# Optimization experiments

Measured on AMD Instinct MI355X. Metric: run time of the kernel, lower is better.

Reference implementation:

```python
import jax, jax.numpy as jnp
from jax import lax
import numpy as np

KS, STRIDE, RATE, SCALE = 3, 1, 2, 10.0  # module init kwargs


def _resize_bilinear_ac(x, oh, ow):
    # F.interpolate(mode='bilinear', align_corners=True); x: [B,C,H,W]
    H, W = x.shape[2], x.shape[3]
    ys = jnp.linspace(0.0, H - 1.0, oh)
    xs = jnp.linspace(0.0, W - 1.0, ow)
    y0 = jnp.floor(ys).astype(jnp.int32)
    y1 = jnp.minimum(y0 + 1, H - 1)
    wy = (ys - y0)[:, None]
    x0 = jnp.floor(xs).astype(jnp.int32)
    x1 = jnp.minimum(x0 + 1, W - 1)
    wx = xs - x0
    g = lambda yi, xi: x[:, :, yi, :][:, :, :, xi]
    top = g(y0, x0) * (1 - wx) + g(y0, x1) * wx
    bot = g(y1, x0) * (1 - wx) + g(y1, x1) * wx
    return top * (1 - wy) + bot * wy


def _conv3x3(x, w, b):
    y = lax.conv_general_dilated(x, w, (1, 1), ((1, 1), (1, 1)),
                                 dimension_numbers=('NCHW', 'OIHW', 'NCHW'))
    return y + b[None, :, None, None]


def _extract_patches(x, k, s):
    # mirrors extract_patches(): ZeroPad2d(1) when k != 1, then unfold h,w
    if k != 1:
        x = jnp.pad(x, ((0, 0), (0, 0), (1, 1), (1, 1)))
    b, c, h, w = x.shape
    nh = (h - k) // s + 1
    nw = (w - k) // s + 1
    cols = jnp.stack([x[:, :, i:i + s * (nh - 1) + 1:s, j:j + s * (nw - 1) + 1:s]
                      for i in range(k) for j in range(k)], axis=-1)  # [B,C,nh,nw,k*k]
    return cols.reshape(b, c, nh, nw, k, k).transpose(0, 2, 3, 1, 4, 5).reshape(b, nh * nw, c, k, k)


def _instance_norm(x, eps=1e-5):
    mu = x.mean((2, 3), keepdims=True)
    var = ((x - mu) ** 2).mean((2, 3), keepdims=True)
    return (x - mu) * lax.rsqrt(var + eps)


def _conv_transpose(att, w):
    # torch F.conv_transpose2d(att, w, stride=2, padding=1); att [Q,h,w], w [Q,Cout,4,4]
    rhs = jnp.flip(w, (-2, -1)).transpose(1, 0, 2, 3)  # [Cout,Q,4,4]
    return lax.conv_general_dilated(att[None], rhs, (1, 1), ((2, 2), (2, 2)),
                                    lhs_dilation=(2, 2),
                                    dimension_numbers=('NCHW', 'OIHW', 'NCHW'))[0]


def _forward(background, foreground, mask, Wc, bc, Wm, bm, Wf, bf):
    h, w = foreground.shape[2], foreground.shape[3]
    mask64 = _resize_bilinear_ac(mask, h, w)
    fg_c = foreground * (1 - mask64)
    fg_m = foreground * mask64
    bg_c = background * (1 - mask64)
    bg_m = background * mask64
    # ODConv2d(fg, bg) stand-in: plain 3x3 conv on the fused features
    bg_c = _conv3x3(fg_c + bg_c, Wc, bc)
    bg_m = _conv3x3(fg_m + bg_m, Wm, bm)
    x = _conv3x3(bg_c + bg_m, Wf, bf)
    x = _instance_norm(x)
    x = x * jax.nn.sigmoid(x)  # MemoryEfficientSwish
    b = x.shape[0]
    raw_w = _extract_patches(x, 2 * RATE, STRIDE * RATE)       # [B,1024,256,4,4]
    x_down = _resize_bilinear_ac(x, h // RATE, w // RATE)       # [B,256,32,32]
    hd, wd = x_down.shape[2], x_down.shape[3]
    pt = _extract_patches(x_down, KS, STRIDE)                   # [B,1024,256,3,3]
    mask32 = _resize_bilinear_ac(mask64, hd, wd)
    mpt = _extract_patches(mask32, KS, STRIDE)                  # [B,1024,1,3,3]
    mm = (mpt.mean((2, 3, 4)) == 0.0).astype(x.dtype)[:, :, None, None]  # [B,1024,1,1]
    norm = jnp.sqrt((pt * pt).sum((2, 3, 4), keepdims=True))
    w_normed = pt / jnp.maximum(norm, 1e-4)
    # score = F.conv2d(x_down, w_normed, padding=1): batched patch-attention GEMM
    score = jnp.einsum('bqckl,bpckl->bqp', w_normed, pt).reshape(b, hd * wd, hd, wd)
    score = score * mm
    att = jax.nn.softmax(score * SCALE, axis=1) * mm
    att = jnp.clip(att, 1e-8, None)
    f1 = jax.vmap(_conv_transpose)(att, raw_w) / 4.0            # [B,256,64,64]
    return f1 * mask64 + x * (1 - mask64)


def setup_inputs() -> dict:
    key = jax.random.key(0)
    ks = jax.random.split(key, 9)
    B, C, H, W = 8, 256, 64, 64
    background = jax.random.normal(ks[0], (B, C, H, W), jnp.float32)
    foreground = jax.random.normal(ks[1], (B, C, H, W), jnp.float32)
    # blocky binary hole mask (16x16 blocks upsampled to 256x256)
    m0 = (jax.random.uniform(ks[2], (B, 1, 16, 16)) > 0.5).astype(jnp.float32)
    mask = jnp.repeat(jnp.repeat(m0, 16, axis=2), 16, axis=3)
    s = 0.05
    Wc = jax.random.normal(ks[3], (256, 256, 3, 3), jnp.float32) * s
    bc = jax.random.normal(ks[4], (256,), jnp.float32) * s
    Wm = jax.random.normal(ks[5], (256, 256, 3, 3), jnp.float32) * s
    bm = jax.random.normal(ks[6], (256,), jnp.float32) * s
    Wf = jax.random.normal(ks[7], (256, 256, 3, 3), jnp.float32) * s
    bf = jax.random.normal(ks[8], (256,), jnp.float32) * s
    return {'background': background, 'foreground': foreground, 'mask': mask,
            'Wc': Wc, 'bc': bc, 'Wm': Wm, 'bm': bm, 'Wf': Wf, 'bf': bf}


def reference(background, foreground, mask, Wc, bc, Wm, bm, Wf, bf):
    return _forward(background, foreground, mask, Wc, bc, Wm, bm, Wf, bf)
```

## Files before the change

### kernel.cpp

```cpp
#include <hip/hip_runtime.h>
#include <math.h>

#define B_ 8
#define C_ 256
#define NPIX 4096
#define NP 1024

typedef __attribute__((ext_vector_type(8))) short bf16x8;
typedef __attribute__((ext_vector_type(4))) float f32x4;

#define GLL16(src, dst) __builtin_amdgcn_global_load_lds( \
    (__attribute__((address_space(1))) void*)(src), \
    (__attribute__((address_space(3))) void*)(dst), 16, 0, 0)

__device__ __forceinline__ unsigned short f2bf(float f) {
  unsigned int u = __float_as_uint(f);
  unsigned int r = (u + 0x7FFFu + ((u >> 16) & 1u)) >> 16;
  return (unsigned short)r;
}
__device__ __forceinline__ unsigned int pk2(unsigned short lo, unsigned short hi) {
  return (unsigned int)lo | ((unsigned int)hi << 16);
}

__device__ __forceinline__ float wave_reduce_sum(float v) {
#pragma unroll
  for (int off = 32; off > 0; off >>= 1) v += __shfl_down(v, off, 64);
  return v;
}
__device__ __forceinline__ float wave_reduce_max(float v) {
#pragma unroll
  for (int off = 32; off > 0; off >>= 1) v = fmaxf(v, __shfl_down(v, off, 64));
  return v;
}

__global__ __launch_bounds__(256) void k_resize(const float* __restrict__ in, float* __restrict__ out,
                                                int IH, int IW, int OH, int OW, int nElem) {
  int idx = blockIdx.x * 256 + threadIdx.x;
  if (idx >= nElem) return;
  int ox = idx % OW; int t = idx / OW; int oy = t % OH; int bc = t / OH;
  float dy = (float)(IH - 1) / (float)(OH - 1);
  float dx = (float)(IW - 1) / (float)(OW - 1);
  float yf = (float)oy * dy;
  float xf = (float)ox * dx;
  float y0f = floorf(yf), x0f = floorf(xf);
  int y0 = (int)y0f, x0 = (int)x0f;
  int y1 = min(y0 + 1, IH - 1), x1 = min(x0 + 1, IW - 1);
  float wy = yf - y0f, wx = xf - x0f;
  const float* p = in + (size_t)bc * IH * IW;
  float a = p[y0 * IW + x0], b = p[y0 * IW + x1];
  float c = p[y1 * IW + x0], d = p[y1 * IW + x1];
  float top = a * (1.0f - wx) + b * wx;
  float bot = c * (1.0f - wx) + d * wx;
  out[idx] = top * (1.0f - wy) + bot * wy;
}

__global__ __launch_bounds__(256) void k_wprep(const float* __restrict__ Wc, const float* __restrict__ Wm,
                                               const float* __restrict__ Wf,
                                               unsigned short* __restrict__ Wp1, unsigned short* __restrict__ Wp2) {
  int idx = blockIdx.x * 256 + threadIdx.x;
  if (idx >= 3 * 589824) return;
  int part = idx / 589824;
  int rem = idx % 589824;
  int kk = rem >> 16, co = (rem >> 8) & 255, ci = rem & 255;
  const float* W = (part == 0) ? Wc : (part == 1) ? Wm : Wf;
  unsigned short o = f2bf(W[(size_t)co * 2304 + ci * 9 + kk]);
  if (part == 0) Wp1[rem] = o;
  else if (part == 1) Wp1[589824 + rem] = o;
  else Wp2[rem] = o;
}

__global__ __launch_bounds__(256) void k_bias(const float* __restrict__ bc, const float* __restrict__ bm,
                                              float* __restrict__ bias1, float* __restrict__ zpg) {
  int i = threadIdx.x;
  bias1[i] = bc[i] + bm[i];
  for (int j = i; j < 2048; j += 256) zpg[j] = 0.f;
}

__global__ __launch_bounds__(256) void k_prepAT(const float* __restrict__ fg, const float* __restrict__ bg,
                                                const float* __restrict__ m64,
                                                unsigned short* __restrict__ A0t, unsigned short* __restrict__ A1t) {
  __shared__ unsigned short T0[64][66];
  __shared__ unsigned short T1[64][66];
  int pt = blockIdx.x, ct = blockIdx.y, b = blockIdx.z;
  int pix0 = pt << 6, ci0 = ct << 6;
  int tid = threadIdx.x;
  {
    int r = tid >> 2, c4 = (tid & 3) << 4;
    size_t ib = (((size_t)(b * 256 + ci0 + r)) << 12) + pix0 + c4;
    const float* fb = fg + ib;
    const float* gb = bg + ib;
    const float* mb = m64 + (((size_t)b) << 12) + pix0 + c4;
#pragma unroll
    for (int k = 0; k < 16; k += 4) {
      float4 f = *(const float4*)(fb + k);
      float4 g = *(const float4*)(gb + k);
      float4 m = *(const float4*)(mb + k);
      float s0 = f.x + g.x, s1 = f.y + g.y, s2 = f.z + g.z, s3 = f.w + g.w;
      T0[r][c4 + k + 0] = f2bf(s0 * (1.f - m.x));
      T0[r][c4 + k + 1] = f2bf(s1 * (1.f - m.y));
      T0[r][c4 + k + 2] = f2bf(s2 * (1.f - m.z));
      T0[r][c4 + k + 3] = f2bf(s3 * (1.f - m.w));
      T1[r][c4 + k + 0] = f2bf(s0 * m.x);
      T1[r][c4 + k + 1] = f2bf(s1 * m.y);
      T1[r][c4 + k + 2] = f2bf(s2 * m.z);
      T1[r][c4 + k + 3] = f2bf(s3 * m.w);
    }
  }
  __syncthreads();
  {
    int pr = tid >> 2, cc = (tid & 3) << 4;
    unsigned int o0[8], o1[8];
#pragma unroll
    for (int k = 0; k < 8; k++) {
      o0[k] = pk2(T0[cc + 2 * k][pr], T0[cc + 2 * k + 1][pr]);
      o1[k] = pk2(T1[cc + 2 * k][pr], T1[cc + 2 * k + 1][pr]);
    }
    size_t ob = ((((size_t)b << 12) + pix0 + pr) << 8) + ci0 + cc;
    *(uint4*)&A0t[ob] = *(uint4*)&o0[0];
    *(uint4*)&A0t[ob + 8] = *(uint4*)&o0[4];
    *(uint4*)&A1t[ob] = *(uint4*)&o1[0];
    *(uint4*)&A1t[ob + 8] = *(uint4*)&o1[4];
  }
}

__device__ __forceinline__ int swz(int row, int slot) {
  return row * 32 + ((slot ^ (row & 3) ^ ((row >> 2) & 3)) << 3);
}

template <int NKK, bool OUT_TRANS_BF16>
__global__ __launch_bounds__(256, 2) void k_conv2ph(const unsigned short* __restrict__ A0t,
                                                    const unsigned short* __restrict__ A1t,
                                                    const unsigned short* __restrict__ Wp,
                                                    const float* __restrict__ bias,
                                                    const unsigned short* __restrict__ zp,
                                                    void* __restrict__ outp) {
  __shared__ __align__(16) unsigned short AB[2][8192];
  int wgl = blockIdx.x + 32 * (blockIdx.y + 2 * blockIdx.z);
  int nid = (wgl & 7) * 64 + (wgl >> 3);
  int bp = nid & 31, cot = (nid >> 5) & 1, b = nid >> 6;
  int tid = threadIdx.x, lane = tid & 63, w3 = tid >> 6;
  int wm = w3 >> 1, wn = w3 & 1;

  int rA = w3 * 32 + (lane >> 2), rA1 = rA + 16;
  int ds0 = (lane & 3) ^ (rA & 3) ^ ((rA >> 2) & 3);
  int ds1 = (lane & 3) ^ (rA1 & 3) ^ ((rA1 >> 2) & 3);
  int y_0 = bp * 2 + (rA >> 6), x_0 = rA & 63;
  int y_1 = bp * 2 + (rA1 >> 6), x_1 = rA1 & 63;
  int co_0 = cot * 128 + rA, co_1 = cot * 128 + rA1;

  f32x4 acc[4][4];
#pragma unroll
  for (int i = 0; i < 4; i++)
#pragma unroll
    for (int j = 0; j < 4; j++) acc[i][j] = (f32x4){0.f, 0.f, 0.f, 0.f};

  const unsigned short *pA0, *pA1, *pB0, *pB1;

#define UPDATE(kkv) {                                                           \
    int kk_ = (kkv);                                                            \
    int kw_ = (NKK == 18 && kk_ >= 9) ? kk_ - 9 : kk_;                          \
    const unsigned short* Asrc_ = (NKK == 18 && kk_ >= 9) ? A1t : A0t;          \
    int ky_ = kw_ / 3 - 1, kx_ = kw_ % 3 - 1;                                   \
    int yy0_ = y_0 + ky_, xx0_ = x_0 + kx_;                                     \
    int yy1_ = y_1 + ky_, xx1_ = x_1 + kx_;                                     \
    pA0 = ((unsigned)yy0_ < 64u && (unsigned)xx0_ < 64u)                        \
        ? Asrc_ + ((((size_t)(b << 6) + yy0_) << 6) + xx0_) * 256 + ds0 * 8     \
        : zp + ds0 * 8;                                                         \
    pA1 = ((unsigned)yy1_ < 64u && (unsigned)xx1_ < 64u)                        \
        ? Asrc_ + ((((size_t)(b << 6) + yy1_) << 6) + xx1_) * 256 + ds1 * 8     \
        : zp + ds1 * 8;                                                         \
    pB0 = Wp + ((size_t)kk_ << 16) + co_0 * 256 + ds0 * 8;                      \
    pB1 = Wp + ((size_t)kk_ << 16) + co_1 * 256 + ds1 * 8;                      \
  }
#define STAGE(c2, buf) {                                                        \
    int ci0_ = ((c2) & 7) << 5;                                                 \
    unsigned short* lb_ = &AB[buf][0];                                          \
    GLL16(pA0 + ci0_, lb_ + w3 * 1024);                                         \
    GLL16(pA1 + ci0_, lb_ + w3 * 1024 + 512);                                   \
    GLL16(pB0 + ci0_, lb_ + 4096 + w3 * 1024);                                  \
    GLL16(pB1 + ci0_, lb_ + 4096 + w3 * 1024 + 512);                            \
  }

  const int NCH = NKK * 8;
  UPDATE(0);
  STAGE(0, 0);
  for (int c = 0; c < NCH; ++c) {
    asm volatile("" ::: "memory");
    __builtin_amdgcn_s_barrier();
    asm volatile("" ::: "memory");
    if (c < NCH - 1) {
      int cn = c + 1;
      if ((cn & 7) == 0) UPDATE(cn >> 3);
      STAGE(cn, cn & 1);
      asm volatile("s_waitcnt vmcnt(4)" ::: "memory");
    } else {
      asm volatile("s_waitcnt vmcnt(0)" ::: "memory");
    }
    __builtin_amdgcn_s_barrier();
    asm volatile("" ::: "memory");
    const unsigned short* Al = &AB[c & 1][0];
    const unsigned short* Bl = &AB[c & 1][4096];
    int slot = lane >> 4;
    int mr = wm * 64 + (lane & 15), ncc = wn * 64 + (lane & 15);
    bf16x8 af[4], bfr[4];
#pragma unroll
    for (int i = 0; i < 4; i++) af[i] = *(const bf16x8*)&Al[swz(mr + i * 16, slot)];
#pragma unroll
    for (int j = 0; j < 4; j++) bfr[j] = *(const bf16x8*)&Bl[swz(ncc + j * 16, slot)];
#pragma unroll
    for (int i = 0; i < 4; i++)
#pragma unroll
      for (int j = 0; j < 4; j++)
        acc[i][j] = __builtin_amdgcn_mfma_f32_16x16x32_bf16(af[i], bfr[j], acc[i][j], 0, 0, 0);
  }
#undef STAGE
#undef UPDATE

  int px0 = bp * 128 + wm * 64 + ((lane >> 4) << 2);
  int co0 = cot * 128 + wn * 64 + (lane & 15);
#pragma unroll
  for (int j = 0; j < 4; j++) {
    int co = co0 + j * 16;
    float bs = bias[co];
#pragma unroll
    for (int i = 0; i < 4; i++) {
#pragma unroll
      for (int r = 0; r < 4; r++) {
        float v = acc[i][j][r] + bs;
        int pix = px0 + i * 16 + r;
        if (OUT_TRANS_BF16)
          ((unsigned short*)outp)[((((size_t)b << 12) + pix) << 8) + co] = f2bf(v);
        else
          ((float*)outp)[((((size_t)b << 8) + co) << 12) + pix] = v;
      }
    }
  }
}

__global__ __launch_bounds__(256) void k_innorm(float* __restrict__ x) {
  __shared__ float s4[4];
  int bc = blockIdx.x;
  float* p = x + (size_t)bc * NPIX;
  int tid = threadIdx.x;
  int lane = tid & 63, w = tid >> 6;
  float v[16];
  float s = 0.f;
#pragma unroll
  for (int i = 0; i < 16; i++) { v[i] = p[tid + i * 256]; s += v[i]; }
  s = wave_reduce_sum(s);
  if (lane == 0) s4[w] = s;
  __syncthreads();
  float mean = (s4[0] + s4[1] + s4[2] + s4[3]) * (1.0f / 4096.0f);
  __syncthreads();
  float s2 = 0.f;
#pragma unroll
  for (int i = 0; i < 16; i++) { float d = v[i] - mean; s2 += d * d; }
  s2 = wave_reduce_sum(s2);
  if (lane == 0) s4[w] = s2;
  __syncthreads();
  float var = (s4[0] + s4[1] + s4[2] + s4[3]) * (1.0f / 4096.0f);
  float inv = 1.0f / sqrtf(var + 1e-5f);
#pragma unroll
  for (int i = 0; i < 16; i++) {
    float xn = (v[i] - mean) * inv;
    float sg = 1.0f / (1.0f + expf(-xn));
    p[tid + i * 256] = xn * sg;
  }
}

__global__ __launch_bounds__(256) void k_trans_xd(const float* __restrict__ xd,
                                                  unsigned short* __restrict__ xdt) {
  __shared__ unsigned short T[64][66];
  int qt = blockIdx.x, ct = blockIdx.y, b = blockIdx.z;
  int q0 = qt << 6, ci0 = ct << 6;
  int tid = threadIdx.x;
  {
    int r = tid >> 2, c4 = (tid & 3) << 4;
    const float* xb = xd + (((size_t)(b * 256 + ci0 + r)) << 10) + q0 + c4;
#pragma unroll
    for (int k = 0; k < 16; k += 4) {
      float4 f = *(const float4*)(xb + k);
      T[r][c4 + k + 0] = f2bf(f.x);
      T[r][c4 + k + 1] = f2bf(f.y);
      T[r][c4 + k + 2] = f2bf(f.z);
      T[r][c4 + k + 3] = f2bf(f.w);
    }
  }
  __syncthreads();
  {
    int qr = tid >> 2, cc = (tid & 3) << 4;
    unsigned int o[8];
#pragma unroll
    for (int k = 0; k < 8; k++) o[k] = pk2(T[cc + 2 * k][qr], T[cc + 2 * k + 1][qr]);
    size_t ob = ((((size_t)b << 10) + q0 + qr) << 8) + ci0 + cc;
    *(uint4*)&xdt[ob] = *(uint4*)&o[0];
    *(uint4*)&xdt[ob + 8] = *(uint4*)&o[4];
  }
}

__global__ __launch_bounds__(256) void k_sq32(const float* __restrict__ xd, float* __restrict__ sq) {
  int idx = blockIdx.x * 256 + threadIdx.x;
  if (idx >= B_ * NP) return;
  int pix = idx & 1023; int b = idx >> 10;
  const float* p = xd + (size_t)b * C_ * NP + pix;
  float s = 0.f;
  for (int c = 0; c < C_; c++) { float v = p[c * NP]; s += v * v; }
  sq[idx] = s;
}

__global__ __launch_bounds__(256) void k_normmm(const float* __restrict__ sq, const float* __restrict__ m32,
                                                float* __restrict__ fq) {
  int idx = blockIdx.x * 256 + threadIdx.x;
  if (idx >= B_ * NP) return;
  int q = idx & 1023, b = idx >> 10;
  int qi = q >> 5, qj = q & 31;
  float ns = 0.f, ms = 0.f;
#pragma unroll
  for (int k = 0; k < 3; k++)
#pragma unroll
    for (int l = 0; l < 3; l++) {
      int r = qi + k - 1, c = qj + l - 1;
      if (r >= 0 && r < 32 && c >= 0 && c < 32) {
        ns += sq[b * NP + r * 32 + c];
        ms += m32[b * NP + r * 32 + c];
      }
    }
  float f = (ms == 0.0f) ? (1.0f / fmaxf(sqrtf(ns), 1e-4f)) : 0.0f;
  fq[idx] = f;
}

__global__ __launch_bounds__(256, 2) void k_gram2ph(const unsigned short* __restrict__ xdt,
                                                    const float* __restrict__ fq,
                                                    const unsigned short* __restrict__ zp,
                                                    float* __restrict__ sc) {
  __shared__ __align__(16) unsigned short AB[2][8192];
  int wgl = blockIdx.x + 8 * (blockIdx.y + 8 * blockIdx.z);
  int nid = (wgl & 7) * 64 + (wgl >> 3);
  int bp = nid & 7, bq = (nid >> 3) & 7, b = nid >> 6;
  int tid = threadIdx.x, lane = tid & 63, w3 = tid >> 6;
  int wm = w3 >> 1, wn = w3 & 1;

  int rA = w3 * 32 + (lane >> 2), rA1 = rA + 16;
  int ds0 = (lane & 3) ^ (rA & 3) ^ ((rA >> 2) & 3);
  int ds1 = (lane & 3) ^ (rA1 & 3) ^ ((rA1 >> 2) & 3);
  int pA0r = bp * 128 + rA, pA1r = bp * 128 + rA1;
  int pB0r = bq * 128 + rA, pB1r = bq * 128 + rA1;
  int piA0 = pA0r >> 5, pjA0 = pA0r & 31, piA1 = pA1r >> 5, pjA1 = pA1r & 31;
  int piB0 = pB0r >> 5, pjB0 = pB0r & 31, piB1 = pB1r >> 5, pjB1 = pB1r & 31;
  const unsigned short* xb = xdt + (((size_t)b) << 18);

  f32x4 acc[4][4];
#pragma unroll
  for (int i = 0; i < 4; i++)
#pragma unroll
    for (int j = 0; j < 4; j++) acc[i][j] = (f32x4){0.f, 0.f, 0.f, 0.f};

  const unsigned short *pA0, *pA1, *pB0, *pB1;

#define GUPDATE(kkv) {                                                          \
    int kk_ = (kkv);                                                            \
    int dy_ = kk_ / 3 - 1, dx_ = kk_ % 3 - 1;                                   \
    int ya0 = piA0 + dy_, xa0 = pjA0 + dx_;                                     \
    int ya1 = piA1 + dy_, xa1 = pjA1 + dx_;                                     \
    int yb0 = piB0 + dy_, xb0 = pjB0 + dx_;                                     \
    int yb1 = piB1 + dy_, xb1 = pjB1 + dx_;                                     \
    pA0 = ((unsigned)ya0 < 32u && (unsigned)xa0 < 32u)                          \
        ? xb + ((((size_t)ya0 << 5) + xa0) << 8) + ds0 * 8 : zp + ds0 * 8;      \
    pA1 = ((unsigned)ya1 < 32u && (unsigned)xa1 < 32u)                          \
        ? xb + ((((size_t)ya1 << 5) + xa1) << 8) + ds1 * 8 : zp + ds1 * 8;      \
    pB0 = ((unsigned)yb0 < 32u && (unsigned)xb0 < 32u)                          \
        ? xb + ((((size_t)yb0 << 5) + xb0) << 8) + ds0 * 8 : zp + ds0 * 8;      \
    pB1 = ((unsigned)yb1 < 32u && (unsigned)xb1 < 32u)                          \
        ? xb + ((((size_t)yb1 << 5) + xb1) << 8) + ds1 * 8 : zp + ds1 * 8;      \
  }
#define GSTAGE(c2, buf) {                                                       \
    int ci0_ = ((c2) & 7) << 5;                                                 \
    unsigned short* lb_ = &AB[buf][0];                                          \
    GLL16(pA0 + ci0_, lb_ + w3 * 1024);                                         \
    GLL16(pA1 + ci0_, lb_ + w3 * 1024 + 512);                                   \
    GLL16(pB0 + ci0_, lb_ + 4096 + w3 * 1024);                                  \
    GLL16(pB1 + ci0_, lb_ + 4096 + w3 * 1024 + 512);                            \
  }

  GUPDATE(0);
  GSTAGE(0, 0);
  for (int c = 0; c < 72; ++c) {
    asm volatile("" ::: "memory");
    __builtin_amdgcn_s_barrier();
    asm volatile("" ::: "memory");
    if (c < 71) {
      int cn = c + 1;
      if ((cn & 7) == 0) GUPDATE(cn >> 3);
      GSTAGE(cn, cn & 1);
      asm volatile("s_waitcnt vmcnt(4)" ::: "memory");
    } else {
      asm volatile("s_waitcnt vmcnt(0)" ::: "memory");
    }
    __builtin_amdgcn_s_barrier();
    asm volatile("" ::: "memory");
    const unsigned short* Al = &AB[c & 1][0];
    const unsigned short* Bl = &AB[c & 1][4096];
    int slot = lane >> 4;
    int mr = wm * 64 + (lane & 15), ncc = wn * 64 + (lane & 15);
    bf16x8 af[4], bfr[4];
#pragma unroll
    for (int i = 0; i < 4; i++) af[i] = *(const bf16x8*)&Al[swz(mr + i * 16, slot)];
#pragma unroll
    for (int j = 0; j < 4; j++) bfr[j] = *(const bf16x8*)&Bl[swz(ncc + j * 16, slot)];
#pragma unroll
    for (int i = 0; i < 4; i++)
#pragma unroll
      for (int j = 0; j < 4; j++)
        acc[i][j] = __builtin_amdgcn_mfma_f32_16x16x32_bf16(af[i], bfr[j], acc[i][j], 0, 0, 0);
  }
#undef GSTAGE
#undef GUPDATE

  int q0 = bq * 128 + wn * 64 + (lane & 15);
  int p0 = bp * 128 + wm * 64 + ((lane >> 4) << 2);
#pragma unroll
  for (int j = 0; j < 4; j++) {
    int q = q0 + j * 16;
    float f = fq[(b << 10) + q];
#pragma unroll
    for (int i = 0; i < 4; i++)
#pragma unroll
      for (int r = 0; r < 4; r++)
        sc[((size_t)(b << 10) + (p0 + i * 16 + r)) * NP + q] = acc[i][j][r] * f;
  }
}

__global__ __launch_bounds__(256) void k_softmax(const float* __restrict__ sc, const float* __restrict__ fq,
                                                 unsigned short* __restrict__ attb) {
  __shared__ float s4[4];
  int row = blockIdx.x;
  int b = row >> 10;
  const float* r = sc + (size_t)row * NP;
  int tid = threadIdx.x;
  int lane = tid & 63, w = tid >> 6;
  float4 sv = *(const float4*)&r[tid * 4];
  float l0 = sv.x * 10.f, l1 = sv.y * 10.f, l2 = sv.z * 10.f, l3 = sv.w * 10.f;
  float mx = fmaxf(fmaxf(l0, l1), fmaxf(l2, l3));
  mx = wave_reduce_max(mx);
  if (lane == 0) s4[w] = mx;
  __syncthreads();
  float M = fmaxf(fmaxf(s4[0], s4[1]), fmaxf(s4[2], s4[3]));
  __syncthreads();
  float e0 = expf(l0 - M), e1 = expf(l1 - M), e2 = expf(l2 - M), e3 = expf(l3 - M);
  float s = e0 + e1 + e2 + e3;
  s = wave_reduce_sum(s);
  if (lane == 0) s4[w] = s;
  __syncthreads();
  float inv = 1.0f / (s4[0] + s4[1] + s4[2] + s4[3]);
  const float* fb = fq + b * NP + tid * 4;
  float m0 = fb[0] > 0.f ? 1.f : 0.f;
  float m1 = fb[1] > 0.f ? 1.f : 0.f;
  float m2 = fb[2] > 0.f ? 1.f : 0.f;
  float m3 = fb[3] > 0.f ? 1.f : 0.f;
  float a0 = fmaxf(e0 * inv * m0, 1e-8f);
  float a1 = fmaxf(e1 * inv * m1, 1e-8f);
  float a2 = fmaxf(e2 * inv * m2, 1e-8f);
  float a3 = fmaxf(e3 * inv * m3, 1e-8f);
  uint2 o;
  o.x = pk2(f2bf(a0), f2bf(a1));
  o.y = pk2(f2bf(a2), f2bf(a3));
  *(uint2*)&attb[(size_t)row * NP + tid * 4] = o;
}

__global__ __launch_bounds__(256) void k_xprep(const float* __restrict__ x,
                                               unsigned short* __restrict__ P0,
                                               unsigned short* __restrict__ P1,
                                               unsigned short* __restrict__ P2) {
  int idx = blockIdx.x * 256 + threadIdx.x;
  int xh8 = idx & 3;
  int yh = (idx >> 2) & 31;
  int co = (idx >> 7) & 255;
  int pc = (idx >> 15) & 3;
  int b  = idx >> 17;
  int cy = pc >> 1, cx = pc & 1;
  const float* row = x + ((size_t)(b * 256 + co) * 64 + (2 * yh + cy)) * 64 + 16 * xh8;
  float4 f0 = *(const float4*)(row);
  float4 f1 = *(const float4*)(row + 4);
  float4 f2 = *(const float4*)(row + 8);
  float4 f3 = *(const float4*)(row + 12);
  unsigned short v0 = f2bf(cx ? f0.y : f0.x), v1 = f2bf(cx ? f0.w : f0.z);
  unsigned short v2 = f2bf(cx ? f1.y : f1.x), v3 = f2bf(cx ? f1.w : f1.z);
  unsigned short v4 = f2bf(cx ? f2.y : f2.x), v5 = f2bf(cx ? f2.w : f2.z);
  unsigned short v6 = f2bf(cx ? f3.y : f3.x), v7 = f2bf(cx ? f3.w : f3.z);
  int prev = __shfl_up((int)v7, 1, 64);
  int next = __shfl_down((int)v0, 1, 64);
  unsigned short pv = (xh8 == 0) ? (unsigned short)0 : (unsigned short)prev;
  unsigned short nx = (xh8 == 3) ? (unsigned short)0 : (unsigned short)next;
  size_t base = ((size_t)((b * 4 + pc) * 256 + co) * 32 + yh) * 32 + 8 * xh8;
  uint4 w0 = {pk2(v0, v1), pk2(v2, v3), pk2(v4, v5), pk2(v6, v7)};
  *(uint4*)&P0[base] = w0;
  uint4 w1 = {pk2(pv, v0), pk2(v1, v2), pk2(v3, v4), pk2(v5, v6)};
  *(uint4*)&P1[base] = w1;
  uint4 w2 = {pk2(v1, v2), pk2(v3, v4), pk2(v5, v6), pk2(v7, nx)};
  *(uint4*)&P2[base] = w2;
}

__global__ __launch_bounds__(256, 2) void k_pv(const unsigned short* __restrict__ attb,
                                               const unsigned short* __restrict__ P0,
                                               const unsigned short* __restrict__ P1,
                                               const unsigned short* __restrict__ P2,
                                               const unsigned short* __restrict__ zp,
                                               const float* __restrict__ xbuf,
                                               const float* __restrict__ m64,
                                               float* __restrict__ out) {
  __shared__ __align__(16) unsigned short AB[2][8192];
  int wg = blockIdx.x + blockIdx.y * 8 + blockIdx.z * 16;
  int nid = (wg & 7) * 64 + (wg >> 3);
  int bn = nid & 7, bm = (nid >> 3) & 1, z = nid >> 4;
  int b = z >> 2, cls = z & 3, cy = cls >> 1, cx = cls & 1;
  int tid = threadIdx.x, lane = tid & 63, w3 = tid >> 6;
  int wm = w3 >> 1, wn = w3 & 1;

  int dy1 = cy ? -1 : 1;
  int pio1 = cy ? 1 : -1;
  int pjo1 = cx ? 1 : -1;
  const unsigned short* Pdx = cx ? P1 : P2;

  int rA0 = w3 * 32 + (lane >> 2);
  int rA1 = rA0 + 16;
  int ds0 = (lane & 3) ^ (rA0 & 3) ^ ((rA0 >> 2) & 3);
  int ds1 = (lane & 3) ^ (rA1 & 3) ^ ((rA1 >> 2) & 3);
  int offA0 = ((z * 256 + bm * 128 + rA0) << 10) + ds0 * 8;
  int offA1 = ((z * 256 + bm * 128 + rA1) << 10) + ds1 * 8;

  const unsigned short* attB = attb + ((size_t)b << 20);
  int o0 = bn * 128 + rA0, o1 = bn * 128 + rA1;
  int oy0 = o0 >> 5, ox0 = o0 & 31, oy1 = o1 >> 5, ox1 = o1 & 31;
#define BPTR(oyv, oxv, dsv, tyv, txv) ({                                        \
    int pi = (oyv) + ((tyv) ? pio1 : 0);                                        \
    int pj = (oxv) + ((txv) ? pjo1 : 0);                                        \
    (pi >= 0 && pi < 32 && pj >= 0 && pj < 32)                                  \
        ? attB + (((pi << 5) + pj) << 10) + (dsv) * 8 : zp; })
  const unsigned short* b0t0 = BPTR(oy0, ox0, ds0, 0, 0);
  const unsigned short* b0t1 = BPTR(oy0, ox0, ds0, 0, 1);
  const unsigned short* b0t2 = BPTR(oy0, ox0, ds0, 1, 0);
  const unsigned short* b0t3 = BPTR(oy0, ox0, ds0, 1, 1);
  const unsigned short* b1t0 = BPTR(oy1, ox1, ds1, 0, 0);
  const unsigned short* b1t1 = BPTR(oy1, ox1, ds1, 0, 1);
  const unsigned short* b1t2 = BPTR(oy1, ox1, ds1, 1, 0);
  const unsigned short* b1t3 = BPTR(oy1, ox1, ds1, 1, 1);
#undef BPTR

  f32x4 acc[4][4];
#pragma unroll
  for (int i = 0; i < 4; i++)
#pragma unroll
    for (int j = 0; j < 4; j++) acc[i][j] = (f32x4){0.f, 0.f, 0.f, 0.f};

  int dA0 = w3 * 1024, dA1 = w3 * 1024 + 512;
  int dB0 = 4096 + w3 * 1024, dB1 = 4096 + w3 * 1024 + 512;

#define PSTAGE(c2, buf) {                                                       \
    int t2 = (c2) >> 5, qi = (c2) & 31;                                         \
    int q32 = qi * 32;                                                          \
    const unsigned short* Ab = (t2 & 1) ? Pdx : P0;                             \
    int dyo = (t2 >> 1) ? dy1 * 32 : 0;                                         \
    bool vA = (t2 < 2) || ((dy1 > 0) ? (qi < 31) : (qi > 0));                   \
    if (!vA) Ab = zp;                                                           \
    int oA0 = vA ? offA0 + dyo + q32 : 0;                                       \
    int oA1 = vA ? offA1 + dyo + q32 : 0;                                       \
    unsigned short* lb = &AB[buf][0];                                           \
    GLL16(Ab + oA0, lb + dA0);                                                  \
    GLL16(Ab + oA1, lb + dA1);                                                  \
    const unsigned short* sB0 = (t2 == 0 ? b0t0 : t2 == 1 ? b0t1 : t2 == 2 ? b0t2 : b0t3) + q32; \
    const unsigned short* sB1 = (t2 == 0 ? b1t0 : t2 == 1 ? b1t1 : t2 == 2 ? b1t2 : b1t3) + q32; \
    GLL16(sB0, lb + dB0);                                                       \
    GLL16(sB1, lb + dB1);                                                       \
  }

  PSTAGE(0, 0);
  for (int c = 0; c < 128; ++c) {
    asm volatile("" ::: "memory");
    __builtin_amdgcn_s_barrier();
    asm volatile("" ::: "memory");
    if (c < 127) {
      PSTAGE(c + 1, (c + 1) & 1);
      asm volatile("s_waitcnt vmcnt(4)" ::: "memory");
    } else {
      asm volatile("s_waitcnt vmcnt(0)" ::: "memory");
    }
    __builtin_amdgcn_s_barrier();
    asm volatile("" ::: "memory");
    const unsigned short* Al = &AB[c & 1][0];
    const unsigned short* Bl = &AB[c & 1][4096];
    int slot = lane >> 4;
    int mr = wm * 64 + (lane & 15), ncc = wn * 64 + (lane & 15);
    bf16x8 af[4], bfr[4];
#pragma unroll
    for (int i = 0; i < 4; i++) af[i] = *(const bf16x8*)&Al[swz(mr + i * 16, slot)];
#pragma unroll
    for (int j = 0; j < 4; j++) bfr[j] = *(const bf16x8*)&Bl[swz(ncc + j * 16, slot)];
#pragma unroll
    for (int i = 0; i < 4; i++)
#pragma unroll
      for (int j = 0; j < 4; j++)
        acc[i][j] = __builtin_amdgcn_mfma_f32_16x16x32_bf16(af[i], bfr[j], acc[i][j], 0, 0, 0);
  }
#undef PSTAGE

  int co0 = bm * 128 + wm * 64 + ((lane >> 4) << 2);
  int oo0 = bn * 128 + wn * 64 + (lane & 15);
#pragma unroll
  for (int j = 0; j < 4; j++) {
    int o = oo0 + j * 16;
    int oy = ((o >> 5) << 1) + cy, ox = ((o & 31) << 1) + cx;
    int opix = oy * 64 + ox;
    float msk = m64[b * NPIX + opix];
    float s = 0.25f * msk, t1m = 1.0f - msk;
#pragma unroll
    for (int i = 0; i < 4; i++) {
#pragma unroll
      for (int r = 0; r < 4; r++) {
        int co = co0 + i * 16 + r;
        size_t xi = (size_t)(b * C_ + co) * NPIX + opix;
        out[xi] = acc[i][j][r] * s + xbuf[xi] * t1m;
      }
    }
  }
}

extern "C" void kernel_launch(void* const* d_in, const int* in_sizes, int n_in,
                              void* d_out, int out_size, void* d_ws, size_t ws_size,
                              hipStream_t stream) {
  const float* bg   = (const float*)d_in[0];
  const float* fg   = (const float*)d_in[1];
  const float* mask = (const float*)d_in[2];
  const float* Wc   = (const float*)d_in[3];
  const float* bc   = (const float*)d_in[4];
  const float* Wm   = (const float*)d_in[5];
  const float* bm   = (const float*)d_in[6];
  const float* Wf   = (const float*)d_in[7];
  const float* bf   = (const float*)d_in[8];
  float* out = (float*)d_out;
  float* w = (float*)d_ws;

  float* mask64 = w;
  float* mask32 = w + 32768;
  float* sq32   = w + 40960;
  float* fq     = w + 49152;
  float* bias1  = w + 57344;
  float* zpage  = w + 57600;
  unsigned short* A0t = (unsigned short*)(w + 65536);
  unsigned short* A1t = (unsigned short*)(w + 65536 + 4194304);
  float* sc = w + 65536;
  unsigned short* P0u = (unsigned short*)(w + 65536);
  unsigned short* P1u = (unsigned short*)(w + 4259840);
  unsigned short* tbuf_t = (unsigned short*)(w + 8454144);
  float* xd = w + 8454144;
  unsigned short* xdt = (unsigned short*)(w + 10551296);
  unsigned short* attb = (unsigned short*)(w + 8454144);
  float* xbuf = w + 12648448;
  unsigned short* Wp1 = (unsigned short*)(w + 21037056);
  unsigned short* Wp2 = (unsigned short*)(w + 21626880);
  unsigned short* P2u = (unsigned short*)(w + 21037056);

  const unsigned short* zp = (const unsigned short*)zpage;

  hipLaunchKernelGGL(k_resize, dim3(128), dim3(256), 0, stream, mask, mask64, 256, 256, 64, 64, 32768);
  hipLaunchKernelGGL(k_wprep, dim3(6912), dim3(256), 0, stream, Wc, Wm, Wf, Wp1, Wp2);
  hipLaunchKernelGGL(k_bias, dim3(1), dim3(256), 0, stream, bc, bm, bias1, zpage);
  hipLaunchKernelGGL(k_prepAT, dim3(64, 4, 8), dim3(256), 0, stream, fg, bg, mask64, A0t, A1t);
  hipLaunchKernelGGL((k_conv2ph<18, true>), dim3(32, 2, 8), dim3(256), 0, stream,
                     A0t, A1t, Wp1, bias1, zp, (void*)tbuf_t);
  hipLaunchKernelGGL((k_conv2ph<9, false>), dim3(32, 2, 8), dim3(256), 0, stream,
                     tbuf_t, tbuf_t, Wp2, bf, zp, (void*)xbuf);
  hipLaunchKernelGGL(k_innorm, dim3(B_ * C_), dim3(256), 0, stream, xbuf);
  hipLaunchKernelGGL(k_resize, dim3(8192), dim3(256), 0, stream, xbuf, xd, 64, 64, 32, 32, B_ * C_ * NP);
  hipLaunchKernelGGL(k_resize, dim3(32), dim3(256), 0, stream, mask64, mask32, 64, 64, 32, 32, B_ * NP);
  hipLaunchKernelGGL(k_trans_xd, dim3(16, 4, 8), dim3(256), 0, stream, xd, xdt);
  hipLaunchKernelGGL(k_sq32, dim3(32), dim3(256), 0, stream, xd, sq32);
  hipLaunchKernelGGL(k_normmm, dim3(32), dim3(256), 0, stream, sq32, mask32, fq);
  hipLaunchKernelGGL(k_gram2ph, dim3(8, 8, 8), dim3(256), 0, stream, xdt, fq, zp, sc);
  hipLaunchKernelGGL(k_softmax, dim3(B_ * NP), dim3(256), 0, stream, sc, fq, attb);
  hipLaunchKernelGGL(k_xprep, dim3(4096), dim3(256), 0, stream, xbuf, P0u, P1u, P2u);
  hipLaunchKernelGGL(k_pv, dim3(8, 2, 32), dim3(256), 0, stream, attb, P0u, P1u, P2u,
                     zp, xbuf, mask64, out);
}
```

Before: 356.1 us.

## Enlarge MFMA GEMM tiles to 256x128 and fuse norm with downsample

The conv, gram and PV GEMM kernels now use 256x128 output tiles, with 8x4 MFMA accumulators per wave and larger LDS stages, in place of 128x128. This halves the workgroup count and raises operand reuse per LDS load. The instance-norm kernel now also does the 64->32 bilinear downsample from shared memory, and the mask downsample is folded into the fq kernel, which removes two launches and one pass over memory. The cost is higher register pressure and fewer workgroups, 256 per GEMM, which may underfill the GPU's compute units.

```diff
diff --git a/kernel.cpp b/kernel.cpp
--- a/kernel.cpp
+++ b/kernel.cpp
@@ -12,6 +12,8 @@
 #define GLL16(src, dst) __builtin_amdgcn_global_load_lds( \
     (__attribute__((address_space(1))) void*)(src), \
     (__attribute__((address_space(3))) void*)(dst), 16, 0, 0)
+
+#define MFMA16(a, b, c) __builtin_amdgcn_mfma_f32_16x16x32_bf16((a), (b), (c), 0, 0, 0)
 
 __device__ __forceinline__ unsigned short f2bf(float f) {
   unsigned int u = __float_as_uint(f);
@@ -127,103 +129,114 @@
   return row * 32 + ((slot ^ (row & 3) ^ ((row >> 2) & 3)) << 3);
 }
 
+
 template <int NKK, bool OUT_TRANS_BF16>
-__global__ __launch_bounds__(256, 2) void k_conv2ph(const unsigned short* __restrict__ A0t,
-                                                    const unsigned short* __restrict__ A1t,
-                                                    const unsigned short* __restrict__ Wp,
-                                                    const float* __restrict__ bias,
-                                                    const unsigned short* __restrict__ zp,
-                                                    void* __restrict__ outp) {
-  __shared__ __align__(16) unsigned short AB[2][8192];
-  int wgl = blockIdx.x + 32 * (blockIdx.y + 2 * blockIdx.z);
-  int nid = (wgl & 7) * 64 + (wgl >> 3);
-  int bp = nid & 31, cot = (nid >> 5) & 1, b = nid >> 6;
+__global__ __launch_bounds__(256, 2) void k_conv3(const unsigned short* __restrict__ A0t,
+                                                  const unsigned short* __restrict__ A1t,
+                                                  const unsigned short* __restrict__ Wp,
+                                                  const float* __restrict__ bias,
+                                                  const unsigned short* __restrict__ zp,
+                                                  void* __restrict__ outp) {
+  __shared__ __align__(16) unsigned short AB[2][12288];
+  int wgl = blockIdx.x;
+  int nid = (wgl & 7) * 32 + (wgl >> 3);
+  int bp = nid & 15, cot = (nid >> 4) & 1, b = nid >> 5;
   int tid = threadIdx.x, lane = tid & 63, w3 = tid >> 6;
   int wm = w3 >> 1, wn = w3 & 1;
 
-  int rA = w3 * 32 + (lane >> 2), rA1 = rA + 16;
-  int ds0 = (lane & 3) ^ (rA & 3) ^ ((rA >> 2) & 3);
-  int ds1 = (lane & 3) ^ (rA1 & 3) ^ ((rA1 >> 2) & 3);
-  int y_0 = bp * 2 + (rA >> 6), x_0 = rA & 63;
-  int y_1 = bp * 2 + (rA1 >> 6), x_1 = rA1 & 63;
-  int co_0 = cot * 128 + rA, co_1 = cot * 128 + rA1;
-
-  f32x4 acc[4][4];
-#pragma unroll
-  for (int i = 0; i < 4; i++)
+  int r0 = w3 * 32 + (lane >> 2), r1 = r0 + 16;
+  int ds0 = (lane & 3) ^ (r0 & 3) ^ ((r0 >> 2) & 3);
+  int ds1 = (lane & 3) ^ (r1 & 3) ^ ((r1 >> 2) & 3);
+  int y0r = bp * 4 + (r0 >> 6), x0r = r0 & 63;
+  int y1r = bp * 4 + (r1 >> 6), x1r = r1 & 63;
+  int y2r = bp * 4 + ((r0 + 128) >> 6), x2r = x0r;
+  int y3r = bp * 4 + ((r1 + 128) >> 6), x3r = x1r;
+  int rb0 = w3 * 16 + (lane >> 2);
+  int dsb = (lane & 3) ^ (rb0 & 3) ^ ((rb0 >> 2) & 3);
+  int cob0 = cot * 128 + rb0, cob1 = cob0 + 64;
+
+  f32x4 acc[8][4];
+#pragma unroll
+  for (int i = 0; i < 8; i++)
 #pragma unroll
     for (int j = 0; j < 4; j++) acc[i][j] = (f32x4){0.f, 0.f, 0.f, 0.f};
 
-  const unsigned short *pA0, *pA1, *pB0, *pB1;
-
-#define UPDATE(kkv) {                                                           \
+  const unsigned short *pA0, *pA1, *pA2, *pA3, *pB0, *pB1;
+#define UPD(kkv) {                                                              \
     int kk_ = (kkv);                                                            \
     int kw_ = (NKK == 18 && kk_ >= 9) ? kk_ - 9 : kk_;                          \
     const unsigned short* Asrc_ = (NKK == 18 && kk_ >= 9) ? A1t : A0t;          \
     int ky_ = kw_ / 3 - 1, kx_ = kw_ % 3 - 1;                                   \
-    int yy0_ = y_0 + ky_, xx0_ = x_0 + kx_;                                     \
-    int yy1_ = y_1 + ky_, xx1_ = x_1 + kx_;                                     \
-    pA0 = ((unsigned)yy0_ < 64u && (unsigned)xx0_ < 64u)                        \
-        ? Asrc_ + ((((size_t)(b << 6) + yy0_) << 6) + xx0_) * 256 + ds0 * 8     \
-        : zp + ds0 * 8;                                                         \
-    pA1 = ((unsigned)yy1_ < 64u && (unsigned)xx1_ < 64u)                        \
-        ? Asrc_ + ((((size_t)(b << 6) + yy1_) << 6) + xx1_) * 256 + ds1 * 8     \
-        : zp + ds1 * 8;                                                         \
-    pB0 = Wp + ((size_t)kk_ << 16) + co_0 * 256 + ds0 * 8;                      \
-    pB1 = Wp + ((size_t)kk_ << 16) + co_1 * 256 + ds1 * 8;                      \
+    int yy, xx;                                                                 \
+    yy = y0r + ky_; xx = x0r + kx_;                                             \
+    pA0 = ((unsigned)yy < 64u && (unsigned)xx < 64u)                            \
+        ? Asrc_ + ((((size_t)(b << 6) + yy) << 6) + xx) * 256 + ds0 * 8 : zp + ds0 * 8; \
+    yy = y1r + ky_; xx = x1r + kx_;                                             \
+    pA1 = ((unsigned)yy < 64u && (unsigned)xx < 64u)                            \
+        ? Asrc_ + ((((size_t)(b << 6) + yy) << 6) + xx) * 256 + ds1 * 8 : zp + ds1 * 8; \
+    yy = y2r + ky_; xx = x2r + kx_;                                             \
+    pA2 = ((unsigned)yy < 64u && (unsigned)xx < 64u)                            \
+        ? Asrc_ + ((((size_t)(b << 6) + yy) << 6) + xx) * 256 + ds0 * 8 : zp + ds0 * 8; \
+    yy = y3r + ky_; xx = x3r + kx_;                                             \
+    pA3 = ((unsigned)yy < 64u && (unsigned)xx < 64u)                            \
+        ? Asrc_ + ((((size_t)(b << 6) + yy) << 6) + xx) * 256 + ds1 * 8 : zp + ds1 * 8; \
+    pB0 = Wp + ((size_t)kk_ << 16) + (size_t)cob0 * 256 + dsb * 8;              \
+    pB1 = Wp + ((size_t)kk_ << 16) + (size_t)cob1 * 256 + dsb * 8;              \
   }
 #define STAGE(c2, buf) {                                                        \
     int ci0_ = ((c2) & 7) << 5;                                                 \
     unsigned short* lb_ = &AB[buf][0];                                          \
     GLL16(pA0 + ci0_, lb_ + w3 * 1024);                                         \
     GLL16(pA1 + ci0_, lb_ + w3 * 1024 + 512);                                   \
-    GLL16(pB0 + ci0_, lb_ + 4096 + w3 * 1024);                                  \
-    GLL16(pB1 + ci0_, lb_ + 4096 + w3 * 1024 + 512);                            \
+    GLL16(pA2 + ci0_, lb_ + 4096 + w3 * 1024);                                  \
+    GLL16(pA3 + ci0_, lb_ + 4096 + w3 * 1024 + 512);                            \
+    GLL16(pB0 + ci0_, lb_ + 8192 + w3 * 512);                                   \
+    GLL16(pB1 + ci0_, lb_ + 8192 + 2048 + w3 * 512);                            \
   }
 
   const int NCH = NKK * 8;
-  UPDATE(0);
+  UPD(0);
   STAGE(0, 0);
+  int slot = lane >> 4;
+  int mr = wm * 128 + (lane & 15), ncc = wn * 64 + (lane & 15);
   for (int c = 0; c < NCH; ++c) {
     asm volatile("" ::: "memory");
     __builtin_amdgcn_s_barrier();
     asm volatile("" ::: "memory");
     if (c < NCH - 1) {
       int cn = c + 1;
-      if ((cn & 7) == 0) UPDATE(cn >> 3);
+      if ((cn & 7) == 0) UPD(cn >> 3);
       STAGE(cn, cn & 1);
-      asm volatile("s_waitcnt vmcnt(4)" ::: "memory");
+      asm volatile("s_waitcnt vmcnt(6)" ::: "memory");
     } else {
       asm volatile("s_waitcnt vmcnt(0)" ::: "memory");
     }
     __builtin_amdgcn_s_barrier();
     asm volatile("" ::: "memory");
     const unsigned short* Al = &AB[c & 1][0];
-    const unsigned short* Bl = &AB[c & 1][4096];
-    int slot = lane >> 4;
-    int mr = wm * 64 + (lane & 15), ncc = wn * 64 + (lane & 15);
-    bf16x8 af[4], bfr[4];
-#pragma unroll
-    for (int i = 0; i < 4; i++) af[i] = *(const bf16x8*)&Al[swz(mr + i * 16, slot)];
+    const unsigned short* Bl = &AB[c & 1][8192];
+    bf16x8 af[8], bfr[4];
+#pragma unroll
+    for (int i = 0; i < 8; i++) af[i] = *(const bf16x8*)&Al[swz(mr + i * 16, slot)];
 #pragma unroll
     for (int j = 0; j < 4; j++) bfr[j] = *(const bf16x8*)&Bl[swz(ncc + j * 16, slot)];
 #pragma unroll
-    for (int i = 0; i < 4; i++)
+    for (int i = 0; i < 8; i++)
 #pragma unroll
       for (int j = 0; j < 4; j++)
-        acc[i][j] = __builtin_amdgcn_mfma_f32_16x16x32_bf16(af[i], bfr[j], acc[i][j], 0, 0, 0);
+        acc[i][j] = MFMA16(af[i], bfr[j], acc[i][j]);
   }
 #undef STAGE
-#undef UPDATE
-
-  int px0 = bp * 128 + wm * 64 + ((lane >> 4) << 2);
+#undef UPD
+
+  int px0 = bp * 256 + wm * 128 + ((lane >> 4) << 2);
   int co0 = cot * 128 + wn * 64 + (lane & 15);
 #pragma unroll
   for (int j = 0; j < 4; j++) {
     int co = co0 + j * 16;
     float bs = bias[co];
 #pragma unroll
-    for (int i = 0; i < 4; i++) {
+    for (int i = 0; i < 8; i++) {
 #pragma unroll
       for (int r = 0; r < 4; r++) {
         float v = acc[i][j][r] + bs;
@@ -237,7 +250,8 @@
   }
 }
 
-__global__ __launch_bounds__(256) void k_innorm(float* __restrict__ x) {
+__global__ __launch_bounds__(256) void k_post(float* __restrict__ x, float* __restrict__ xd) {
+  __shared__ float sL[4096];
   __shared__ float s4[4];
   int bc = blockIdx.x;
   float* p = x + (size_t)bc * NPIX;
@@ -264,7 +278,28 @@
   for (int i = 0; i < 16; i++) {
     float xn = (v[i] - mean) * inv;
     float sg = 1.0f / (1.0f + expf(-xn));
-    p[tid + i * 256] = xn * sg;
+    float o = xn * sg;
+    p[tid + i * 256] = o;
+    sL[tid + i * 256] = o;
+  }
+  __syncthreads();
+  float dyx = 63.0f / 31.0f;
+  float* xdp = xd + (size_t)bc * NP;
+#pragma unroll
+  for (int k = 0; k < 4; k++) {
+    int q = tid + k * 256;
+    int yq = q >> 5, xq = q & 31;
+    float yf = (float)yq * dyx;
+    float xf = (float)xq * dyx;
+    float y0f = floorf(yf), x0f = floorf(xf);
+    int y0 = (int)y0f, x0 = (int)x0f;
+    int y1 = min(y0 + 1, 63), x1 = min(x0 + 1, 63);
+    float wy = yf - y0f, wx = xf - x0f;
+    float a = sL[y0 * 64 + x0], b2 = sL[y0 * 64 + x1];
+    float c2 = sL[y1 * 64 + x0], d2 = sL[y1 * 64 + x1];
+    float top = a * (1.0f - wx) + b2 * wx;
+    float bot = c2 * (1.0f - wx) + d2 * wx;
+    xdp[q] = top * (1.0f - wy) + bot * wy;
   }
 }
 
@@ -308,12 +343,14 @@
   sq[idx] = s;
 }
 
-__global__ __launch_bounds__(256) void k_normmm(const float* __restrict__ sq, const float* __restrict__ m32,
-                                                float* __restrict__ fq) {
+__global__ __launch_bounds__(256) void k_fq(const float* __restrict__ sq, const float* __restrict__ m64,
+                                            float* __restrict__ fq) {
   int idx = blockIdx.x * 256 + threadIdx.x;
   if (idx >= B_ * NP) return;
   int q = idx & 1023, b = idx >> 10;
   int qi = q >> 5, qj = q & 31;
+  const float* mb = m64 + (b << 12);
+  float dyx = 63.0f / 31.0f;
   float ns = 0.f, ms = 0.f;
 #pragma unroll
   for (int k = 0; k < 3; k++)
@@ -322,108 +359,129 @@
       int r = qi + k - 1, c = qj + l - 1;
       if (r >= 0 && r < 32 && c >= 0 && c < 32) {
         ns += sq[b * NP + r * 32 + c];
-        ms += m32[b * NP + r * 32 + c];
+        float yf = (float)r * dyx, xf = (float)c * dyx;
+        float y0f = floorf(yf), x0f = floorf(xf);
+        int y0 = (int)y0f, x0 = (int)x0f;
+        int y1 = min(y0 + 1, 63), x1 = min(x0 + 1, 63);
+        float wy = yf - y0f, wx = xf - x0f;
+        float a = mb[y0 * 64 + x0], b2 = mb[y0 * 64 + x1];
+        float c2 = mb[y1 * 64 + x0], d2 = mb[y1 * 64 + x1];
+        float top = a * (1.0f - wx) + b2 * wx;
+        float bot = c2 * (1.0f - wx) + d2 * wx;
+        ms += top * (1.0f - wy) + bot * wy;
       }
     }
   float f = (ms == 0.0f) ? (1.0f / fmaxf(sqrtf(ns), 1e-4f)) : 0.0f;
   fq[idx] = f;
 }
 
-__global__ __launch_bounds__(256, 2) void k_gram2ph(const unsigned short* __restrict__ xdt,
-                                                    const float* __restrict__ fq,
-                                                    const unsigned short* __restrict__ zp,
-                                                    float* __restrict__ sc) {
-  __shared__ __align__(16) unsigned short AB[2][8192];
-  int wgl = blockIdx.x + 8 * (blockIdx.y + 8 * blockIdx.z);
-  int nid = (wgl & 7) * 64 + (wgl >> 3);
-  int bp = nid & 7, bq = (nid >> 3) & 7, b = nid >> 6;
+__global__ __launch_bounds__(256, 2) void k_gram3(const unsigned short* __restrict__ xdt,
+                                                  const float* __restrict__ fq,
+                                                  const unsigned short* __restrict__ zp,
+                                                  float* __restrict__ sc) {
+  __shared__ __align__(16) unsigned short AB[2][12288];
+  int wgl = blockIdx.x;
+  int nid = (wgl & 7) * 32 + (wgl >> 3);
+  int bq = nid & 7, bp = (nid >> 3) & 3, b = nid >> 5;
   int tid = threadIdx.x, lane = tid & 63, w3 = tid >> 6;
   int wm = w3 >> 1, wn = w3 & 1;
 
-  int rA = w3 * 32 + (lane >> 2), rA1 = rA + 16;
-  int ds0 = (lane & 3) ^ (rA & 3) ^ ((rA >> 2) & 3);
-  int ds1 = (lane & 3) ^ (rA1 & 3) ^ ((rA1 >> 2) & 3);
-  int pA0r = bp * 128 + rA, pA1r = bp * 128 + rA1;
-  int pB0r = bq * 128 + rA, pB1r = bq * 128 + rA1;
-  int piA0 = pA0r >> 5, pjA0 = pA0r & 31, piA1 = pA1r >> 5, pjA1 = pA1r & 31;
-  int piB0 = pB0r >> 5, pjB0 = pB0r & 31, piB1 = pB1r >> 5, pjB1 = pB1r & 31;
+  int r0 = w3 * 32 + (lane >> 2), r1 = r0 + 16;
+  int ds0 = (lane & 3) ^ (r0 & 3) ^ ((r0 >> 2) & 3);
+  int ds1 = (lane & 3) ^ (r1 & 3) ^ ((r1 >> 2) & 3);
+  int rb0 = w3 * 16 + (lane >> 2);
+  int dsb = (lane & 3) ^ (rb0 & 3) ^ ((rb0 >> 2) & 3);
+
+  int pr0 = bp * 256 + r0, pr1 = bp * 256 + r1, pr2 = pr0 + 128, pr3 = pr1 + 128;
+  int qr0 = bq * 128 + rb0, qr1 = qr0 + 64;
+  int pi0 = pr0 >> 5, pj0 = pr0 & 31, pi1 = pr1 >> 5, pj1 = pr1 & 31;
+  int pi2 = pr2 >> 5, pj2 = pr2 & 31, pi3 = pr3 >> 5, pj3 = pr3 & 31;
+  int qi0 = qr0 >> 5, qj0 = qr0 & 31, qi1 = qr1 >> 5, qj1 = qr1 & 31;
   const unsigned short* xb = xdt + (((size_t)b) << 18);
 
-  f32x4 acc[4][4];
-#pragma unroll
-  for (int i = 0; i < 4; i++)
+  f32x4 acc[8][4];
+#pragma unroll
+  for (int i = 0; i < 8; i++)
 #pragma unroll
     for (int j = 0; j < 4; j++) acc[i][j] = (f32x4){0.f, 0.f, 0.f, 0.f};
 
-  const unsigned short *pA0, *pA1, *pB0, *pB1;
-
-#define GUPDATE(kkv) {                                                          \
+  const unsigned short *pA0, *pA1, *pA2, *pA3, *pB0, *pB1;
+#define GUPD(kkv) {                                                             \
     int kk_ = (kkv);                                                            \
     int dy_ = kk_ / 3 - 1, dx_ = kk_ % 3 - 1;                                   \
-    int ya0 = piA0 + dy_, xa0 = pjA0 + dx_;                                     \
-    int ya1 = piA1 + dy_, xa1 = pjA1 + dx_;                                     \
-    int yb0 = piB0 + dy_, xb0 = pjB0 + dx_;                                     \
-    int yb1 = piB1 + dy_, xb1 = pjB1 + dx_;                                     \
-    pA0 = ((unsigned)ya0 < 32u && (unsigned)xa0 < 32u)                          \
-        ? xb + ((((size_t)ya0 << 5) + xa0) << 8) + ds0 * 8 : zp + ds0 * 8;      \
-    pA1 = ((unsigned)ya1 < 32u && (unsigned)xa1 < 32u)                          \
-        ? xb + ((((size_t)ya1 << 5) + xa1) << 8) + ds1 * 8 : zp + ds1 * 8;      \
-    pB0 = ((unsigned)yb0 < 32u && (unsigned)xb0 < 32u)                          \
-        ? xb + ((((size_t)yb0 << 5) + xb0) << 8) + ds0 * 8 : zp + ds0 * 8;      \
-    pB1 = ((unsigned)yb1 < 32u && (unsigned)xb1 < 32u)                          \
-        ? xb + ((((size_t)yb1 << 5) + xb1) << 8) + ds1 * 8 : zp + ds1 * 8;      \
+    int yy, xx;                                                                 \
+    yy = pi0 + dy_; xx = pj0 + dx_;                                             \
+    pA0 = ((unsigned)yy < 32u && (unsigned)xx < 32u)                            \
+        ? xb + ((((size_t)yy << 5) + xx) << 8) + ds0 * 8 : zp + ds0 * 8;        \
+    yy = pi1 + dy_; xx = pj1 + dx_;                                             \
+    pA1 = ((unsigned)yy < 32u && (unsigned)xx < 32u)                            \
+        ? xb + ((((size_t)yy << 5) + xx) << 8) + ds1 * 8 : zp + ds1 * 8;        \
+    yy = pi2 + dy_; xx = pj2 + dx_;                                             \
+    pA2 = ((unsigned)yy < 32u && (unsigned)xx < 32u)                            \
+        ? xb + ((((size_t)yy << 5) + xx) << 8) + ds0 * 8 : zp + ds0 * 8;        \
+    yy = pi3 + dy_; xx = pj3 + dx_;                                             \
+    pA3 = ((unsigned)yy < 32u && (unsigned)xx < 32u)                            \
+        ? xb + ((((size_t)yy << 5) + xx) << 8) + ds1 * 8 : zp + ds1 * 8;        \
+    yy = qi0 + dy_; xx = qj0 + dx_;                                             \
+    pB0 = ((unsigned)yy < 32u && (unsigned)xx < 32u)                            \
+        ? xb + ((((size_t)yy << 5) + xx) << 8) + dsb * 8 : zp + dsb * 8;        \
+    yy = qi1 + dy_; xx = qj1 + dx_;                                             \
+    pB1 = ((unsigned)yy < 32u && (unsigned)xx < 32u)                            \
+        ? xb + ((((size_t)yy << 5) + xx) << 8) + dsb * 8 : zp + dsb * 8;        \
   }
 #define GSTAGE(c2, buf) {                                                       \
     int ci0_ = ((c2) & 7) << 5;                                                 \
     unsigned short* lb_ = &AB[buf][0];                                          \
     GLL16(pA0 + ci0_, lb_ + w3 * 1024);                                         \
     GLL16(pA1 + ci0_, lb_ + w3 * 1024 + 512);                                   \
-    GLL16(pB0 + ci0_, lb_ + 4096 + w3 * 1024);                                  \
-    GLL16(pB1 + ci0_, lb_ + 4096 + w3 * 1024 + 512);                            \
-  }
-
-  GUPDATE(0);
+    GLL16(pA2 + ci0_, lb_ + 4096 + w3 * 1024);                                  \
+    GLL16(pA3 + ci0_, lb_ + 4096 + w3 * 1024 + 512);                            \
+    GLL16(pB0 + ci0_, lb_ + 8192 + w3 * 512);                                   \
+    GLL16(pB1 + ci0_, lb_ + 8192 + 2048 + w3 * 512);                            \
+  }
+
+  GUPD(0);
   GSTAGE(0, 0);
+  int slot = lane >> 4;
+  int mr = wm * 128 + (lane & 15), ncc = wn * 64 + (lane & 15);
   for (int c = 0; c < 72; ++c) {
     asm volatile("" ::: "memory");
     __builtin_amdgcn_s_barrier();
     asm volatile("" ::: "memory");
     if (c < 71) {
       int cn = c + 1;
-      if ((cn & 7) == 0) GUPDATE(cn >> 3);
+      if ((cn & 7) == 0) GUPD(cn >> 3);
       GSTAGE(cn, cn & 1);
-      asm volatile("s_waitcnt vmcnt(4)" ::: "memory");
+      asm volatile("s_waitcnt vmcnt(6)" ::: "memory");
     } else {
       asm volatile("s_waitcnt vmcnt(0)" ::: "memory");
     }
     __builtin_amdgcn_s_barrier();
     asm volatile("" ::: "memory");
     const unsigned short* Al = &AB[c & 1][0];
-    const unsigned short* Bl = &AB[c & 1][4096];
-    int slot = lane >> 4;
-    int mr = wm * 64 + (lane & 15), ncc = wn * 64 + (lane & 15);
-    bf16x8 af[4], bfr[4];
-#pragma unroll
-    for (int i = 0; i < 4; i++) af[i] = *(const bf16x8*)&Al[swz(mr + i * 16, slot)];
+    const unsigned short* Bl = &AB[c & 1][8192];
+    bf16x8 af[8], bfr[4];
+#pragma unroll
+    for (int i = 0; i < 8; i++) af[i] = *(const bf16x8*)&Al[swz(mr + i * 16, slot)];
 #pragma unroll
     for (int j = 0; j < 4; j++) bfr[j] = *(const bf16x8*)&Bl[swz(ncc + j * 16, slot)];
 #pragma unroll
-    for (int i = 0; i < 4; i++)
+    for (int i = 0; i < 8; i++)
 #pragma unroll
       for (int j = 0; j < 4; j++)
-        acc[i][j] = __builtin_amdgcn_mfma_f32_16x16x32_bf16(af[i], bfr[j], acc[i][j], 0, 0, 0);
+        acc[i][j] = MFMA16(af[i], bfr[j], acc[i][j]);
   }
 #undef GSTAGE
-#undef GUPDATE
+#undef GUPD
 
   int q0 = bq * 128 + wn * 64 + (lane & 15);
-  int p0 = bp * 128 + wm * 64 + ((lane >> 4) << 2);
+  int p0 = bp * 256 + wm * 128 + ((lane >> 4) << 2);
 #pragma unroll
   for (int j = 0; j < 4; j++) {
     int q = q0 + j * 16;
     float f = fq[(b << 10) + q];
 #pragma unroll
-    for (int i = 0; i < 4; i++)
+    for (int i = 0; i < 8; i++)
 #pragma unroll
       for (int r = 0; r < 4; r++)
         sc[((size_t)(b << 10) + (p0 + i * 16 + r)) * NP + q] = acc[i][j][r] * f;
@@ -500,110 +558,112 @@
   *(uint4*)&P2[base] = w2;
 }
 
-__global__ __launch_bounds__(256, 2) void k_pv(const unsigned short* __restrict__ attb,
-                                               const unsigned short* __restrict__ P0,
-                                               const unsigned short* __restrict__ P1,
-                                               const unsigned short* __restrict__ P2,
-                                               const unsigned short* __restrict__ zp,
-                                               const float* __restrict__ xbuf,
-                                               const float* __restrict__ m64,
-                                               float* __restrict__ out) {
-  __shared__ __align__(16) unsigned short AB[2][8192];
-  int wg = blockIdx.x + blockIdx.y * 8 + blockIdx.z * 16;
-  int nid = (wg & 7) * 64 + (wg >> 3);
-  int bn = nid & 7, bm = (nid >> 3) & 1, z = nid >> 4;
+__global__ __launch_bounds__(256, 2) void k_pv3(const unsigned short* __restrict__ attb,
+                                                const unsigned short* __restrict__ P0_,
+                                                const unsigned short* __restrict__ P1,
+                                                const unsigned short* __restrict__ P2,
+                                                const unsigned short* __restrict__ zp,
+                                                const float* __restrict__ xbuf,
+                                                const float* __restrict__ m64,
+                                                float* __restrict__ out) {
+  __shared__ __align__(16) unsigned short AB[2][12288];
+  int wgl = blockIdx.x;
+  int nid = (wgl & 7) * 32 + (wgl >> 3);
+  int bn = nid & 7, z = nid >> 3;
   int b = z >> 2, cls = z & 3, cy = cls >> 1, cx = cls & 1;
   int tid = threadIdx.x, lane = tid & 63, w3 = tid >> 6;
   int wm = w3 >> 1, wn = w3 & 1;
 
   int dy1 = cy ? -1 : 1;
-  int pio1 = cy ? 1 : -1;
-  int pjo1 = cx ? 1 : -1;
+  int pio1 = cy ? 1 : -1, pjo1 = cx ? 1 : -1;
   const unsigned short* Pdx = cx ? P1 : P2;
 
-  int rA0 = w3 * 32 + (lane >> 2);
-  int rA1 = rA0 + 16;
-  int ds0 = (lane & 3) ^ (rA0 & 3) ^ ((rA0 >> 2) & 3);
-  int ds1 = (lane & 3) ^ (rA1 & 3) ^ ((rA1 >> 2) & 3);
-  int offA0 = ((z * 256 + bm * 128 + rA0) << 10) + ds0 * 8;
-  int offA1 = ((z * 256 + bm * 128 + rA1) << 10) + ds1 * 8;
-
+  int r0 = w3 * 32 + (lane >> 2), r1 = r0 + 16;
+  int ds0 = (lane & 3) ^ (r0 & 3) ^ ((r0 >> 2) & 3);
+  int ds1 = (lane & 3) ^ (r1 & 3) ^ ((r1 >> 2) & 3);
+  size_t offA0 = (((size_t)z * 256 + r0) << 10) + ds0 * 8;
+  size_t offA1 = (((size_t)z * 256 + r1) << 10) + ds1 * 8;
+  size_t offA2 = offA0 + ((size_t)128 << 10);
+  size_t offA3 = offA1 + ((size_t)128 << 10);
+
+  int rb0 = w3 * 16 + (lane >> 2);
+  int dsb = (lane & 3) ^ (rb0 & 3) ^ ((rb0 >> 2) & 3);
   const unsigned short* attB = attb + ((size_t)b << 20);
-  int o0 = bn * 128 + rA0, o1 = bn * 128 + rA1;
-  int oy0 = o0 >> 5, ox0 = o0 & 31, oy1 = o1 >> 5, ox1 = o1 & 31;
-#define BPTR(oyv, oxv, dsv, tyv, txv) ({                                        \
+  int oB0 = bn * 128 + rb0, oB1 = oB0 + 64;
+  int oy0 = oB0 >> 5, ox0 = oB0 & 31, oy1 = oB1 >> 5, ox1 = oB1 & 31;
+#define BPTR(oyv, oxv, tyv, txv) ({                                             \
     int pi = (oyv) + ((tyv) ? pio1 : 0);                                        \
     int pj = (oxv) + ((txv) ? pjo1 : 0);                                        \
     (pi >= 0 && pi < 32 && pj >= 0 && pj < 32)                                  \
-        ? attB + (((pi << 5) + pj) << 10) + (dsv) * 8 : zp; })
-  const unsigned short* b0t0 = BPTR(oy0, ox0, ds0, 0, 0);
-  const unsigned short* b0t1 = BPTR(oy0, ox0, ds0, 0, 1);
-  const unsigned short* b0t2 = BPTR(oy0, ox0, ds0, 1, 0);
-  const unsigned short* b0t3 = BPTR(oy0, ox0, ds0, 1, 1);
-  const unsigned short* b1t0 = BPTR(oy1, ox1, ds1, 0, 0);
-  const unsigned short* b1t1 = BPTR(oy1, ox1, ds1, 0, 1);
-  const unsigned short* b1t2 = BPTR(oy1, ox1, ds1, 1, 0);
-  const unsigned short* b1t3 = BPTR(oy1, ox1, ds1, 1, 1);
+        ? attB + (((pi << 5) + pj) << 10) + dsb * 8 : zp + dsb * 8; })
+  const unsigned short* b0t0 = BPTR(oy0, ox0, 0, 0);
+  const unsigned short* b0t1 = BPTR(oy0, ox0, 0, 1);
+  const unsigned short* b0t2 = BPTR(oy0, ox0, 1, 0);
+  const unsigned short* b0t3 = BPTR(oy0, ox0, 1, 1);
+  const unsigned short* b1t0 = BPTR(oy1, ox1, 0, 0);
+  const unsigned short* b1t1 = BPTR(oy1, ox1, 0, 1);
+  const unsigned short* b1t2 = BPTR(oy1, ox1, 1, 0);
+  const unsigned short* b1t3 = BPTR(oy1, ox1, 1, 1);
 #undef BPTR
 
-  f32x4 acc[4][4];
-#pragma unroll
-  for (int i = 0; i < 4; i++)
+  f32x4 acc[8][4];
+#pragma unroll
+  for (int i = 0; i < 8; i++)
 #pragma unroll
     for (int j = 0; j < 4; j++) acc[i][j] = (f32x4){0.f, 0.f, 0.f, 0.f};
-
-  int dA0 = w3 * 1024, dA1 = w3 * 1024 + 512;
-  int dB0 = 4096 + w3 * 1024, dB1 = 4096 + w3 * 1024 + 512;
 
 #define PSTAGE(c2, buf) {                                                       \
     int t2 = (c2) >> 5, qi = (c2) & 31;                                         \
     int q32 = qi * 32;                                                          \
-    const unsigned short* Ab = (t2 & 1) ? Pdx : P0;                             \
+    const unsigned short* Ab = (t2 & 1) ? Pdx : P0_;                            \
     int dyo = (t2 >> 1) ? dy1 * 32 : 0;                                         \
     bool vA = (t2 < 2) || ((dy1 > 0) ? (qi < 31) : (qi > 0));                   \
-    if (!vA) Ab = zp;                                                           \
-    int oA0 = vA ? offA0 + dyo + q32 : 0;                                       \
-    int oA1 = vA ? offA1 + dyo + q32 : 0;                                       \
     unsigned short* lb = &AB[buf][0];                                           \
-    GLL16(Ab + oA0, lb + dA0);                                                  \
-    GLL16(Ab + oA1, lb + dA1);                                                  \
+    const unsigned short* s0 = vA ? Ab + offA0 + dyo + q32 : zp + ds0 * 8;      \
+    const unsigned short* s1 = vA ? Ab + offA1 + dyo + q32 : zp + ds1 * 8;      \
+    const unsigned short* s2 = vA ? Ab + offA2 + dyo + q32 : zp + ds0 * 8;      \
+    const unsigned short* s3 = vA ? Ab + offA3 + dyo + q32 : zp + ds1 * 8;      \
+    GLL16(s0, lb + w3 * 1024);                                                  \
+    GLL16(s1, lb + w3 * 1024 + 512);                                            \
+    GLL16(s2, lb + 4096 + w3 * 1024);                                           \
+    GLL16(s3, lb + 4096 + w3 * 1024 + 512);                                     \
     const unsigned short* sB0 = (t2 == 0 ? b0t0 : t2 == 1 ? b0t1 : t2 == 2 ? b0t2 : b0t3) + q32; \
     const unsigned short* sB1 = (t2 == 0 ? b1t0 : t2 == 1 ? b1t1 : t2 == 2 ? b1t2 : b1t3) + q32; \
-    GLL16(sB0, lb + dB0);                                                       \
-    GLL16(sB1, lb + dB1);                                                       \
+    GLL16(sB0, lb + 8192 + w3 * 512);                                           \
+    GLL16(sB1, lb + 8192 + 2048 + w3 * 512);                                    \
   }
 
   PSTAGE(0, 0);
+  int slot = lane >> 4;
+  int mr = wm * 128 + (lane & 15), ncc = wn * 64 + (lane & 15);
   for (int c = 0; c < 128; ++c) {
     asm volatile("" ::: "memory");
     __builtin_amdgcn_s_barrier();
     asm volatile("" ::: "memory");
     if (c < 127) {
       PSTAGE(c + 1, (c + 1) & 1);
-      asm volatile("s_waitcnt vmcnt(4)" ::: "memory");
+      asm volatile("s_waitcnt vmcnt(6)" ::: "memory");
     } else {
       asm volatile("s_waitcnt vmcnt(0)" ::: "memory");
     }
     __builtin_amdgcn_s_barrier();
     asm volatile("" ::: "memory");
     const unsigned short* Al = &AB[c & 1][0];
-    const unsigned short* Bl = &AB[c & 1][4096];
-    int slot = lane >> 4;
-    int mr = wm * 64 + (lane & 15), ncc = wn * 64 + (lane & 15);
-    bf16x8 af[4], bfr[4];
-#pragma unroll
-    for (int i = 0; i < 4; i++) af[i] = *(const bf16x8*)&Al[swz(mr + i * 16, slot)];
+    const unsigned short* Bl = &AB[c & 1][8192];
+    bf16x8 af[8], bfr[4];
+#pragma unroll
+    for (int i = 0; i < 8; i++) af[i] = *(const bf16x8*)&Al[swz(mr + i * 16, slot)];
 #pragma unroll
     for (int j = 0; j < 4; j++) bfr[j] = *(const bf16x8*)&Bl[swz(ncc + j * 16, slot)];
 #pragma unroll
-    for (int i = 0; i < 4; i++)
+    for (int i = 0; i < 8; i++)
 #pragma unroll
       for (int j = 0; j < 4; j++)
-        acc[i][j] = __builtin_amdgcn_mfma_f32_16x16x32_bf16(af[i], bfr[j], acc[i][j], 0, 0, 0);
+        acc[i][j] = MFMA16(af[i], bfr[j], acc[i][j]);
   }
 #undef PSTAGE
 
-  int co0 = bm * 128 + wm * 64 + ((lane >> 4) << 2);
+  int co0 = wm * 128 + ((lane >> 4) << 2);
   int oo0 = bn * 128 + wn * 64 + (lane & 15);
 #pragma unroll
   for (int j = 0; j < 4; j++) {
@@ -613,7 +673,7 @@
     float msk = m64[b * NPIX + opix];
     float s = 0.25f * msk, t1m = 1.0f - msk;
 #pragma unroll
-    for (int i = 0; i < 4; i++) {
+    for (int i = 0; i < 8; i++) {
 #pragma unroll
       for (int r = 0; r < 4; r++) {
         int co = co0 + i * 16 + r;
@@ -640,7 +700,6 @@
   float* w = (float*)d_ws;
 
   float* mask64 = w;
-  float* mask32 = w + 32768;
   float* sq32   = w + 40960;
   float* fq     = w + 49152;
   float* bias1  = w + 57344;
@@ -665,19 +724,17 @@
   hipLaunchKernelGGL(k_wprep, dim3(6912), dim3(256), 0, stream, Wc, Wm, Wf, Wp1, Wp2);
   hipLaunchKernelGGL(k_bias, dim3(1), dim3(256), 0, stream, bc, bm, bias1, zpage);
   hipLaunchKernelGGL(k_prepAT, dim3(64, 4, 8), dim3(256), 0, stream, fg, bg, mask64, A0t, A1t);
-  hipLaunchKernelGGL((k_conv2ph<18, true>), dim3(32, 2, 8), dim3(256), 0, stream,
+  hipLaunchKernelGGL((k_conv3<18, true>), dim3(256), dim3(256), 0, stream,
                      A0t, A1t, Wp1, bias1, zp, (void*)tbuf_t);
-  hipLaunchKernelGGL((k_conv2ph<9, false>), dim3(32, 2, 8), dim3(256), 0, stream,
+  hipLaunchKernelGGL((k_conv3<9, false>), dim3(256), dim3(256), 0, stream,
                      tbuf_t, tbuf_t, Wp2, bf, zp, (void*)xbuf);
-  hipLaunchKernelGGL(k_innorm, dim3(B_ * C_), dim3(256), 0, stream, xbuf);
-  hipLaunchKernelGGL(k_resize, dim3(8192), dim3(256), 0, stream, xbuf, xd, 64, 64, 32, 32, B_ * C_ * NP);
-  hipLaunchKernelGGL(k_resize, dim3(32), dim3(256), 0, stream, mask64, mask32, 64, 64, 32, 32, B_ * NP);
+  hipLaunchKernelGGL(k_post, dim3(B_ * C_), dim3(256), 0, stream, xbuf, xd);
   hipLaunchKernelGGL(k_trans_xd, dim3(16, 4, 8), dim3(256), 0, stream, xd, xdt);
   hipLaunchKernelGGL(k_sq32, dim3(32), dim3(256), 0, stream, xd, sq32);
-  hipLaunchKernelGGL(k_normmm, dim3(32), dim3(256), 0, stream, sq32, mask32, fq);
-  hipLaunchKernelGGL(k_gram2ph, dim3(8, 8, 8), dim3(256), 0, stream, xdt, fq, zp, sc);
+  hipLaunchKernelGGL(k_fq, dim3(32), dim3(256), 0, stream, sq32, mask64, fq);
+  hipLaunchKernelGGL(k_gram3, dim3(256), dim3(256), 0, stream, xdt, fq, zp, sc);
   hipLaunchKernelGGL(k_softmax, dim3(B_ * NP), dim3(256), 0, stream, sc, fq, attb);
   hipLaunchKernelGGL(k_xprep, dim3(4096), dim3(256), 0, stream, xbuf, P0u, P1u, P2u);
-  hipLaunchKernelGGL(k_pv, dim3(8, 2, 32), dim3(256), 0, stream, attb, P0u, P1u, P2u,
+  hipLaunchKernelGGL(k_pv3, dim3(256), dim3(256), 0, stream, attb, P0u, P1u, P2u,
                      zp, xbuf, mask64, out);
 }
```

New measurement: 415.1 us. 16.6% more time.
